# Performance work log

Hardware: AMD Instinct MI355X
Metric: run time of the kernel (lower is better)

## Reference

```python
import jax, jax.numpy as jnp
import numpy as np

N_SCALES = 5
EPS = 1e-8


def setup_inputs() -> dict:
    key = jax.random.key(0)
    # [B, T] log-return series
    log_returns = jax.random.normal(key, (4096, 8192), dtype=jnp.float32) * 0.01
    return {"log_returns": log_returns}


def _log_rs(x, s):
    """Mean over chunks of the R/S statistic at scale s, in log space.

    x: [B, T] -> returns [B].  Vectorizes the per-chunk loop of the torch
    module by reshaping to [B, n_chunks, s].
    """
    B, T = x.shape
    nc = T // s
    chunks = x[:, : nc * s].reshape(B, nc, s)
    y = chunks - chunks.mean(axis=-1, keepdims=True)
    cs = jnp.cumsum(y, axis=-1)
    R = cs.max(axis=-1) - cs.min(axis=-1)                 # [B, nc]
    S = jnp.maximum(jnp.std(chunks, axis=-1, ddof=1), EPS)  # unbiased std, clamp(min=1e-8)
    rs = jnp.maximum(R / S, EPS)
    return jnp.log(jnp.maximum(rs.mean(axis=-1), EPS))    # [B]


def reference(log_returns):
    x = log_returns
    B, T = x.shape
    # scale schedule is a pure function of the static length T
    min_scale = max(4, T // 2 ** N_SCALES)
    scales = []
    for k in range(N_SCALES):
        s = max(4, min_scale * 2 ** k)
        if s > T // 2:
            break
        scales.append(s)
    # log-log OLS slope: H = Cov(log n, log R/S) / Var(log n)
    ln = jnp.log(jnp.array(scales, dtype=x.dtype))                     # [K]
    lr = jnp.stack([_log_rs(x, s) for s in scales], axis=-1)           # [B, K]
    ln_c = ln - ln.mean()
    lr_c = lr - lr.mean(axis=-1, keepdims=True)
    num = (ln_c * lr_c).sum(axis=-1)
    den = jnp.maximum((ln_c ** 2).sum(), 1e-8)
    return jnp.clip(num / den, 0.05, 0.95)                             # [B]
```

## Files before the change

### kernel.cpp

```cpp
#include <hip/hip_runtime.h>
#include <math.h>

#define TLEN 8192
#define NTH 256

__device__ __forceinline__ int padi(int i) { return i + (i >> 5); }

__global__ __launch_bounds__(NTH) void hurst_kernel(const float* __restrict__ x,
                                                    float* __restrict__ out) {
    __shared__ float Q[TLEN + (TLEN >> 5)];
    __shared__ float wbuf[8];
    __shared__ float SSp[257];
    __shared__ float meanb[32];
    __shared__ float Rbuf[32];
    __shared__ float wred[8];
    __shared__ float lrbuf[8];

    const int t = threadIdx.x;
    const int lane = t & 63;
    const int wave = t >> 6;
    const long long row = blockIdx.x;
    const float* xr = x + row * TLEN;

    #pragma unroll
    for (int j = 0; j < 8; ++j) {
        int p = j * 1024 + t * 4;
        float4 v = *reinterpret_cast<const float4*>(xr + p);
        Q[padi(p + 0)] = v.x;
        Q[padi(p + 1)] = v.y;
        Q[padi(p + 2)] = v.z;
        Q[padi(p + 3)] = v.w;
    }
    __syncthreads();

    float seg[32];
    const int base = t * 33;
    float ssum = 0.f, ssq = 0.f;
    #pragma unroll
    for (int k = 0; k < 32; ++k) {
        float v = Q[base + k];
        seg[k] = v;
        ssum += v;
        ssq += v * v;
    }

    float v1 = ssum, v2 = ssq;
    #pragma unroll
    for (int d = 1; d < 64; d <<= 1) {
        float u1 = __shfl_up(v1, d, 64);
        float u2 = __shfl_up(v2, d, 64);
        if (lane >= d) { v1 += u1; v2 += u2; }
    }
    if (lane == 63) { wbuf[wave] = v1; wbuf[4 + wave] = v2; }
    __syncthreads();
    float woff1 = 0.f, woff2 = 0.f;
    for (int w = 0; w < wave; ++w) { woff1 += wbuf[w]; woff2 += wbuf[4 + w]; }
    const float ex1 = woff1 + v1 - ssum;
    const float ex2 = woff2 + v2 - ssq;
    SSp[t] = ex2;
    if (t == NTH - 1) SSp[256] = ex2 + ssq;

    float run = ex1;
    #pragma unroll
    for (int k = 0; k < 32; ++k) {
        run += seg[k];
        Q[base + k] = run;
    }
    __syncthreads();

    const int p0 = t * 32;
    #pragma unroll
    for (int si = 0; si < 5; ++si) {
        const int s = 256 << si;
        const int nc = TLEN / s;
        const int group = s >> 5;

        if (t < nc) {
            float q1 = Q[padi((t + 1) * s - 1)];
            float q0 = (t > 0) ? Q[padi(t * s - 1)] : 0.f;
            meanb[t] = (q1 - q0) / (float)s;
        }
        __syncthreads();

        const int c = t / group;
        const float m = meanb[c];
        float hmax = -INFINITY, hmin = INFINITY;
        #pragma unroll
        for (int k = 0; k < 32; ++k) {
            float h = Q[base + k] - (float)(p0 + k + 1) * m;
            hmax = fmaxf(hmax, h);
            hmin = fminf(hmin, h);
        }
        #pragma unroll
        for (int w = 1; w < 64; w <<= 1) {
            if (w >= group) break;
            hmax = fmaxf(hmax, __shfl_xor(hmax, w, 64));
            hmin = fminf(hmin, __shfl_xor(hmin, w, 64));
        }
        if (group >= 128) {
            if (lane == 0) { wred[wave] = hmax; wred[4 + wave] = hmin; }
            __syncthreads();
            if (t < nc) {
                float a = fmaxf(wred[2 * t], wred[2 * t + 1]);
                float b = fminf(wred[4 + 2 * t], wred[4 + 2 * t + 1]);
                Rbuf[t] = a - b;
            }
        } else {
            if ((t & (group - 1)) == 0) Rbuf[c] = hmax - hmin;
        }
        __syncthreads();

        float rs = 0.f;
        if (t < nc) {
            float m2 = meanb[t];
            int sg = s >> 5;
            float ss = SSp[(t + 1) * sg] - SSp[t * sg];
            float var = (ss - (float)s * m2 * m2) / (float)(s - 1);
            float S = fmaxf(sqrtf(fmaxf(var, 0.f)), 1e-8f);
            rs = fmaxf(Rbuf[t] / S, 1e-8f);
        }
        if (wave == 0) {
            #pragma unroll
            for (int w = 16; w >= 1; w >>= 1)
                rs += __shfl_down(rs, w, 64);
            if (lane == 0)
                lrbuf[si] = logf(fmaxf(rs / (float)nc, 1e-8f));
        }
        __syncthreads();
    }

    if (t == 0) {
        float num = -2.f * lrbuf[0] - lrbuf[1] + lrbuf[3] + 2.f * lrbuf[4];
        float H = num * (1.0f / (10.0f * 0.69314718055994530942f));
        H = fminf(fmaxf(H, 0.05f), 0.95f);
        out[row] = H;
    }
}

extern "C" void kernel_launch(void* const* d_in, const int* in_sizes, int n_in,
                              void* d_out, int out_size, void* d_ws, size_t ws_size,
                              hipStream_t stream) {
    const float* x = (const float*)d_in[0];
    float* out = (float*)d_out;
    const int B = in_sizes[0] / TLEN;
    hurst_kernel<<<dim3(B), dim3(NTH), 0, stream>>>(x, out);
}
```

Measured before the change: 189.2 us.

## Process row in two halves, keep prefix sums in registers, batch scale reductions

Loads the 8192-element row in two 4096-element halves through a smaller shared buffer, and keeps each thread's 2x16 running prefix sums in registers rather than writing the full cumsum back to shared memory. Chunk means and stds are computed for all five scales at once from per-thread prefix sums, and the per-scale max/min reductions write partials to shared arrays, so there are far fewer block barriers. The aim is to roughly halve LDS use per block so more blocks fit per CU, and to remove the per-scale syncs and shared rereads. In exchange it adds register pressure and an extra barrier for the second half-load.

```diff
diff --git a/kernel.cpp b/kernel.cpp
--- a/kernel.cpp
+++ b/kernel.cpp
@@ -2,138 +2,185 @@
 #include <math.h>
 
 #define TLEN 8192
-#define NTH 256
+#define HALF 4096
+#define NTH  256
 
 __device__ __forceinline__ int padi(int i) { return i + (i >> 5); }
 
 __global__ __launch_bounds__(NTH) void hurst_kernel(const float* __restrict__ x,
                                                     float* __restrict__ out) {
-    __shared__ float Q[TLEN + (TLEN >> 5)];
-    __shared__ float wbuf[8];
-    __shared__ float SSp[257];
-    __shared__ float meanb[32];
-    __shared__ float Rbuf[32];
-    __shared__ float wred[8];
-    __shared__ float lrbuf[8];
+    __shared__ float SB[HALF + (HALF >> 5)];
+    __shared__ float Sp[513];
+    __shared__ float SSp[513];
+    __shared__ float wsum[4], wssq[4];
+    __shared__ float meanL[62], SL[62];
+    __shared__ float pmax[72], pmin[72];
+    __shared__ float rsb[62];
 
     const int t = threadIdx.x;
     const int lane = t & 63;
     const int wave = t >> 6;
-    const long long row = blockIdx.x;
-    const float* xr = x + row * TLEN;
+    const float* xr = x + (long long)blockIdx.x * TLEN;
+
+    float P[2][16];
+    float carry_s = 0.f, carry_q = 0.f;
 
     #pragma unroll
-    for (int j = 0; j < 8; ++j) {
-        int p = j * 1024 + t * 4;
-        float4 v = *reinterpret_cast<const float4*>(xr + p);
-        Q[padi(p + 0)] = v.x;
-        Q[padi(p + 1)] = v.y;
-        Q[padi(p + 2)] = v.z;
-        Q[padi(p + 3)] = v.w;
+    for (int h = 0; h < 2; ++h) {
+        const float* xh = xr + h * HALF;
+        #pragma unroll
+        for (int j = 0; j < 4; ++j) {
+            int p = j * 1024 + t * 4;
+            float4 v = *reinterpret_cast<const float4*>(xh + p);
+            SB[padi(p)]     = v.x;
+            SB[padi(p + 1)] = v.y;
+            SB[padi(p + 2)] = v.z;
+            SB[padi(p + 3)] = v.w;
+        }
+        __syncthreads();
+
+        const int base = 16 * t + (t >> 1);
+        float rr[16];
+        float ssum = 0.f, ssq = 0.f;
+        #pragma unroll
+        for (int k = 0; k < 16; ++k) {
+            float v = SB[base + k];
+            rr[k] = v;
+            ssum += v;
+            ssq = fmaf(v, v, ssq);
+        }
+
+        float v1 = ssum, v2 = ssq;
+        #pragma unroll
+        for (int d = 1; d < 64; d <<= 1) {
+            float u1 = __shfl_up(v1, d, 64);
+            float u2 = __shfl_up(v2, d, 64);
+            if (lane >= d) { v1 += u1; v2 += u2; }
+        }
+        if (lane == 63) { wsum[wave] = v1; wssq[wave] = v2; }
+        __syncthreads();
+        float w0 = wsum[0], w1 = wsum[1], w2 = wsum[2], w3 = wsum[3];
+        float q0 = wssq[0], q1 = wssq[1], q2 = wssq[2], q3 = wssq[3];
+        float woff1 = carry_s, woff2 = carry_q;
+        if (wave > 0) { woff1 += w0; woff2 += q0; }
+        if (wave > 1) { woff1 += w1; woff2 += q1; }
+        if (wave > 2) { woff1 += w2; woff2 += q2; }
+        carry_s += w0 + w1 + w2 + w3;
+        carry_q += q0 + q1 + q2 + q3;
+
+        float ex1 = woff1 + (v1 - ssum);
+        float ex2 = woff2 + (v2 - ssq);
+        Sp[h * 256 + t]  = ex1;
+        SSp[h * 256 + t] = ex2;
+
+        float run = ex1;
+        #pragma unroll
+        for (int k = 0; k < 16; ++k) { run += rr[k]; P[h][k] = run; }
+    }
+    if (t == 0) { Sp[512] = carry_s; SSp[512] = carry_q; }
+    __syncthreads();
+
+    if (t < 62) {
+        int si, ci;
+        if (t < 32)      { si = 0; ci = t; }
+        else if (t < 48) { si = 1; ci = t - 32; }
+        else if (t < 56) { si = 2; ci = t - 48; }
+        else if (t < 60) { si = 3; ci = t - 56; }
+        else             { si = 4; ci = t - 60; }
+        int g = 16 << si;
+        int a = ci * g, b = a + g;
+        float s_f = (float)(256 << si);
+        float sum = Sp[b] - Sp[a];
+        float sq  = SSp[b] - SSp[a];
+        float m = sum / s_f;
+        float var = (sq - s_f * m * m) / (s_f - 1.0f);
+        meanL[t] = m;
+        SL[t] = fmaxf(sqrtf(fmaxf(var, 0.f)), 1e-8f);
     }
     __syncthreads();
 
-    float seg[32];
-    const int base = t * 33;
-    float ssum = 0.f, ssq = 0.f;
     #pragma unroll
-    for (int k = 0; k < 32; ++k) {
-        float v = Q[base + k];
-        seg[k] = v;
-        ssum += v;
-        ssq += v * v;
-    }
+    for (int si = 0; si < 5; ++si) {
+        const int lg = 4 + si;
+        const int g = 1 << lg;
+        const int OFF  = (si == 0) ? 0 : (si == 1) ? 32 : (si == 2) ? 48 : (si == 3) ? 56 : 60;
+        const int POFF = (si == 0) ? 0 : (si == 1) ? 32 : (si == 2) ? 48 : (si == 3) ? 56 : 64;
+        const int c0 = t >> lg;
+        const int c1 = (256 >> lg) + c0;
+        const float m0 = meanL[OFF + c0];
+        const float m1 = meanL[OFF + c1];
 
-    float v1 = ssum, v2 = ssq;
-    #pragma unroll
-    for (int d = 1; d < 64; d <<= 1) {
-        float u1 = __shfl_up(v1, d, 64);
-        float u2 = __shfl_up(v2, d, 64);
-        if (lane >= d) { v1 += u1; v2 += u2; }
-    }
-    if (lane == 63) { wbuf[wave] = v1; wbuf[4 + wave] = v2; }
-    __syncthreads();
-    float woff1 = 0.f, woff2 = 0.f;
-    for (int w = 0; w < wave; ++w) { woff1 += wbuf[w]; woff2 += wbuf[4 + w]; }
-    const float ex1 = woff1 + v1 - ssum;
-    const float ex2 = woff2 + v2 - ssq;
-    SSp[t] = ex2;
-    if (t == NTH - 1) SSp[256] = ex2 + ssq;
+        float mx0 = -INFINITY, mn0 = INFINITY, mx1 = -INFINITY, mn1 = INFINITY;
+        #pragma unroll
+        for (int k = 0; k < 16; ++k) {
+            float g0 = fmaf(-m0, (float)k, P[0][k]);
+            float g1 = fmaf(-m1, (float)k, P[1][k]);
+            mx0 = fmaxf(mx0, g0); mn0 = fminf(mn0, g0);
+            mx1 = fmaxf(mx1, g1); mn1 = fminf(mn1, g1);
+        }
+        const float rb1 = (float)(16 * (t & (g - 1)) + 1);
+        mx0 -= rb1 * m0; mn0 -= rb1 * m0;
+        mx1 -= rb1 * m1; mn1 -= rb1 * m1;
 
-    float run = ex1;
-    #pragma unroll
-    for (int k = 0; k < 32; ++k) {
-        run += seg[k];
-        Q[base + k] = run;
+        const int bw = (g < 64) ? g : 64;
+        #pragma unroll
+        for (int w = 1; w < bw; w <<= 1) {
+            mx0 = fmaxf(mx0, __shfl_xor(mx0, w, 64));
+            mn0 = fminf(mn0, __shfl_xor(mn0, w, 64));
+            mx1 = fmaxf(mx1, __shfl_xor(mx1, w, 64));
+            mn1 = fminf(mn1, __shfl_xor(mn1, w, 64));
+        }
+        if ((t & (bw - 1)) == 0) {
+            const int pc  = (g > 64) ? (g >> 6) : 1;
+            const int sub = (t >> 6) & (pc - 1);
+            pmax[POFF + c0 * pc + sub] = mx0;
+            pmin[POFF + c0 * pc + sub] = mn0;
+            pmax[POFF + c1 * pc + sub] = mx1;
+            pmin[POFF + c1 * pc + sub] = mn1;
+        }
     }
     __syncthreads();
 
-    const int p0 = t * 32;
-    #pragma unroll
-    for (int si = 0; si < 5; ++si) {
-        const int s = 256 << si;
-        const int nc = TLEN / s;
-        const int group = s >> 5;
+    if (t < 62) {
+        int si, ci;
+        if (t < 32)      { si = 0; ci = t; }
+        else if (t < 48) { si = 1; ci = t - 32; }
+        else if (t < 56) { si = 2; ci = t - 48; }
+        else if (t < 60) { si = 3; ci = t - 56; }
+        else             { si = 4; ci = t - 60; }
+        const int pc   = (si == 3) ? 2 : (si == 4) ? 4 : 1;
+        const int POFF = (si == 0) ? 0 : (si == 1) ? 32 : (si == 2) ? 48 : (si == 3) ? 56 : 64;
+        int bsl = POFF + ci * pc;
+        float mx = pmax[bsl], mn = pmin[bsl];
+        #pragma unroll 4
+        for (int j = 1; j < pc; ++j) {
+            mx = fmaxf(mx, pmax[bsl + j]);
+            mn = fminf(mn, pmin[bsl + j]);
+        }
+        float R = mx - mn;
+        rsb[t] = fmaxf(R / SL[t], 1e-8f);
+    }
+    __syncthreads();
 
-        if (t < nc) {
-            float q1 = Q[padi((t + 1) * s - 1)];
-            float q0 = (t > 0) ? Q[padi(t * s - 1)] : 0.f;
-            meanb[t] = (q1 - q0) / (float)s;
+    float lrv = 0.f;
+    if (t < 5) {
+        const int nc  = 32 >> t;
+        const int OFF = (t == 0) ? 0 : (t == 1) ? 32 : (t == 2) ? 48 : (t == 3) ? 56 : 60;
+        float s = 0.f;
+        for (int j = 0; j < nc; ++j) s += rsb[OFF + j];
+        lrv = logf(fmaxf(s / (float)nc, 1e-8f));
+    }
+    if (wave == 0) {
+        float n0 = __shfl(lrv, 0, 64);
+        float n1 = __shfl(lrv, 1, 64);
+        float n3 = __shfl(lrv, 3, 64);
+        float n4 = __shfl(lrv, 4, 64);
+        if (lane == 0) {
+            float H = (-2.f * n0 - n1 + n3 + 2.f * n4)
+                      * (1.0f / (10.0f * 0.69314718055994530942f));
+            H = fminf(fmaxf(H, 0.05f), 0.95f);
+            out[blockIdx.x] = H;
         }
-        __syncthreads();
-
-        const int c = t / group;
-        const float m = meanb[c];
-        float hmax = -INFINITY, hmin = INFINITY;
-        #pragma unroll
-        for (int k = 0; k < 32; ++k) {
-            float h = Q[base + k] - (float)(p0 + k + 1) * m;
-            hmax = fmaxf(hmax, h);
-            hmin = fminf(hmin, h);
-        }
-        #pragma unroll
-        for (int w = 1; w < 64; w <<= 1) {
-            if (w >= group) break;
-            hmax = fmaxf(hmax, __shfl_xor(hmax, w, 64));
-            hmin = fminf(hmin, __shfl_xor(hmin, w, 64));
-        }
-        if (group >= 128) {
-            if (lane == 0) { wred[wave] = hmax; wred[4 + wave] = hmin; }
-            __syncthreads();
-            if (t < nc) {
-                float a = fmaxf(wred[2 * t], wred[2 * t + 1]);
-                float b = fminf(wred[4 + 2 * t], wred[4 + 2 * t + 1]);
-                Rbuf[t] = a - b;
-            }
-        } else {
-            if ((t & (group - 1)) == 0) Rbuf[c] = hmax - hmin;
-        }
-        __syncthreads();
-
-        float rs = 0.f;
-        if (t < nc) {
-            float m2 = meanb[t];
-            int sg = s >> 5;
-            float ss = SSp[(t + 1) * sg] - SSp[t * sg];
-            float var = (ss - (float)s * m2 * m2) / (float)(s - 1);
-            float S = fmaxf(sqrtf(fmaxf(var, 0.f)), 1e-8f);
-            rs = fmaxf(Rbuf[t] / S, 1e-8f);
-        }
-        if (wave == 0) {
-            #pragma unroll
-            for (int w = 16; w >= 1; w >>= 1)
-                rs += __shfl_down(rs, w, 64);
-            if (lane == 0)
-                lrbuf[si] = logf(fmaxf(rs / (float)nc, 1e-8f));
-        }
-        __syncthreads();
-    }
-
-    if (t == 0) {
-        float num = -2.f * lrbuf[0] - lrbuf[1] + lrbuf[3] + 2.f * lrbuf[4];
-        float H = num * (1.0f / (10.0f * 0.69314718055994530942f));
-        H = fminf(fmaxf(H, 0.05f), 0.95f);
-        out[row] = H;
     }
 }
 
```

Result: no change. 191.7 us (+1.3%).
